# Performance work log

Hardware: AMD Instinct MI355X
Metric: run time of the kernel (lower is better)

Reference implementation:

```python
import jax, jax.numpy as jnp
import numpy as np

B, K, C, H, W = 16, 32, 256, 80, 80
NH, HD = 8, 32          # num_heads, head_dim (C = NH*HD)
S = 4                   # fixed roi_align sampling grid per 1x1 output bin
EPS = 1e-5


def _bn(x, g, b, m, v):
    # inference-mode BatchNorm2d, NCHW
    s = g / jnp.sqrt(v + EPS)
    return x * s[None, :, None, None] + (b - m * s)[None, :, None, None]


def _bilinear(feat, ys, xs):
    # feat [B,C,H,W]; ys,xs [B,K,S,S] -> [B,K,S,S,C], torchvision roi_align semantics
    Hh, Ww = feat.shape[2], feat.shape[3]
    valid = (ys >= -1.0) & (ys <= Hh) & (xs >= -1.0) & (xs <= Ww)
    y = jnp.clip(ys, 0.0, Hh - 1.0)
    x = jnp.clip(xs, 0.0, Ww - 1.0)
    y0 = jnp.floor(y); x0 = jnp.floor(x)
    y0i = y0.astype(jnp.int32); x0i = x0.astype(jnp.int32)
    y1i = jnp.minimum(y0i + 1, Hh - 1); x1i = jnp.minimum(x0i + 1, Ww - 1)
    ly = y - y0; lx = x - x0; hy = 1.0 - ly; hx = 1.0 - lx
    bidx = jnp.arange(feat.shape[0])[:, None, None, None]
    g = lambda yi, xi: feat[bidx, :, yi, xi]  # -> [B,K,S,S,C]
    val = ((hy * hx)[..., None] * g(y0i, x0i) + (hy * lx)[..., None] * g(y0i, x1i)
           + (ly * hx)[..., None] * g(y1i, x0i) + (ly * lx)[..., None] * g(y1i, x1i))
    return val * valid[..., None].astype(val.dtype)


def _roi_align_1x1(feat, boxes):
    # boxes [B,K,4] normalized xyxy; spatial_scale = 1.0 in the source
    Hh, Ww = feat.shape[2], feat.shape[3]
    sc = jnp.asarray([Ww - 1, Hh - 1, Ww - 1, Hh - 1], feat.dtype)
    ab = boxes * sc
    x1, y1, x2, y2 = ab[..., 0], ab[..., 1], ab[..., 2], ab[..., 3]
    rw = jnp.maximum(x2 - x1, 1.0)
    rh = jnp.maximum(y2 - y1, 1.0)
    grid = (jnp.arange(S, dtype=feat.dtype) + 0.5) / S
    ys = y1[..., None] + grid * rh[..., None]   # [B,K,S]
    xs = x1[..., None] + grid * rw[..., None]
    ys2, xs2 = jnp.broadcast_arrays(ys[..., :, None], xs[..., None, :])  # [B,K,S,S]
    vals = _bilinear(feat, ys2, xs2)            # [B,K,S,S,C]
    return vals.mean(axis=(2, 3)).reshape(feat.shape[0] * boxes.shape[1], -1)


def _gat(nodes, wq, bq, wk, bkp, wv, bv, scale, wo, bo, ln_g, ln_b):
    Bk = nodes.shape[0]
    q = (nodes @ wq.T + bq).reshape(Bk, NH, HD)
    k = (nodes @ wk.T + bkp).reshape(Bk, NH, HD)
    v = (nodes @ wv.T + bv).reshape(Bk, NH, HD)
    scores = jnp.einsum('ihd,jhd->ijh', q, k) * scale
    attn = jax.nn.softmax(scores, axis=1)       # softmax over keys j
    msg = jnp.einsum('ijh,jhd->ihd', attn, v).reshape(Bk, NH * HD)
    y = nodes + msg @ wo.T + bo
    mu = y.mean(-1, keepdims=True)
    var = ((y - mu) ** 2).mean(-1, keepdims=True)
    return (y - mu) / jnp.sqrt(var + EPS) * ln_g + ln_b


def _forward(x, boxes, conv_w, conv_b, bn1_g, bn1_b, bn1_m, bn1_v,
             wq, bq, wk, bkp, wv, bv, scale, wo, bo, ln_g, ln_b,
             rec_w, rec_b, bn2_g, bn2_b, bn2_m, bn2_v):
    feat = jax.lax.conv_general_dilated(
        x, conv_w, (1, 1), 'SAME',
        dimension_numbers=('NCHW', 'OIHW', 'NCHW')) + conv_b[None, :, None, None]
    feat = _bn(feat, bn1_g, bn1_b, bn1_m, bn1_v)
    feat = feat * jax.nn.sigmoid(feat)          # SiLU
    nodes = _roi_align_1x1(feat, boxes)         # [B*K, C]
    enh = _gat(nodes, wq, bq, wk, bkp, wv, bv, scale, wo, bo, ln_g, ln_b)
    f = enh.reshape(B, K, C)
    wts = jax.nn.softmax(f.mean(-1), axis=1)    # [B,K]
    weighted = jnp.einsum('bkc,bk->bc', f, wts)
    # out map is spatially constant -> 1x1 conv + BN collapse to per-sample affine
    y = weighted @ rec_w[:, :, 0, 0].T + rec_b
    s = bn2_g / jnp.sqrt(bn2_v + EPS)
    y = y * s + (bn2_b - bn2_m * s)
    return x + y[:, :, None, None]


def setup_inputs() -> dict:
    key = jax.random.key(0)
    ks = jax.random.split(key, 10)
    x = jax.random.normal(ks[0], (B, C, H, W), jnp.float32)
    bx = jax.random.uniform(ks[1], (B, K, 4), jnp.float32)
    bx = bx.at[:, :, 2:].add(bx[:, :, :2])      # xy2 += xy1
    boxes = jnp.clip(bx, 0.0, 1.0)
    w = lambda k, shp: jax.random.normal(k, shp, jnp.float32) * 0.02
    return {
        'x': x, 'boxes': boxes,
        'conv_w': w(ks[2], (C, C, 3, 3)), 'conv_b': jnp.zeros((C,), jnp.float32),
        'bn1_g': jnp.ones((C,), jnp.float32), 'bn1_b': jnp.zeros((C,), jnp.float32),
        'bn1_m': jnp.zeros((C,), jnp.float32), 'bn1_v': jnp.ones((C,), jnp.float32),
        'wq': w(ks[3], (C, C)), 'bq': jnp.zeros((C,), jnp.float32),
        'wk': w(ks[4], (C, C)), 'bkp': jnp.zeros((C,), jnp.float32),
        'wv': w(ks[5], (C, C)), 'bv': jnp.zeros((C,), jnp.float32),
        'scale': jnp.asarray(1.0 / np.sqrt(HD), jnp.float32),
        'wo': w(ks[6], (C, C)), 'bo': jnp.zeros((C,), jnp.float32),
        'ln_g': jnp.ones((C,), jnp.float32), 'ln_b': jnp.zeros((C,), jnp.float32),
        'rec_w': w(ks[7], (C, C, 1, 1)), 'rec_b': jnp.zeros((C,), jnp.float32),
        'bn2_g': jnp.ones((C,), jnp.float32), 'bn2_b': jnp.zeros((C,), jnp.float32),
        'bn2_m': jnp.zeros((C,), jnp.float32), 'bn2_v': jnp.ones((C,), jnp.float32),
    }


def reference(x, boxes, conv_w, conv_b, bn1_g, bn1_b, bn1_m, bn1_v,
              wq, bq, wk, bkp, wv, bv, scale, wo, bo, ln_g, ln_b,
              rec_w, rec_b, bn2_g, bn2_b, bn2_m, bn2_v):
    return _forward(x, boxes, conv_w, conv_b, bn1_g, bn1_b, bn1_m, bn1_v,
                    wq, bq, wk, bkp, wv, bv, scale, wo, bo, ln_g, ln_b,
                    rec_w, rec_b, bn2_g, bn2_b, bn2_m, bn2_v)
```

## Files before the change

### kernel.cpp

```cpp
#include <hip/hip_runtime.h>

#define EPSV 1e-5f

typedef __attribute__((ext_vector_type(8))) short short8v;
typedef __attribute__((ext_vector_type(4))) float f32x4;

static __device__ __forceinline__ unsigned short f2bf(float f) {
  unsigned int u = __float_as_uint(f);
  u += 0x7fff + ((u >> 16) & 1);
  return (unsigned short)(u >> 16);
}
static __device__ __forceinline__ float bf2f(unsigned short h) {
  return __uint_as_float(((unsigned int)h) << 16);
}

static __device__ __forceinline__ void glds16(const void* g, void* l) {
  __builtin_amdgcn_global_load_lds(
      (const __attribute__((address_space(1))) void*)g,
      (__attribute__((address_space(3))) void*)l, 16, 0, 0);
}

__global__ __launch_bounds__(256) void prep_fused_kernel(
    const float* __restrict__ x, unsigned short* __restrict__ xin,
    const float* __restrict__ cw, unsigned short* __restrict__ Wr,
    float* __restrict__ zpad,
    const float* __restrict__ wq, const float* __restrict__ wk,
    const float* __restrict__ wv, const float* __restrict__ wo,
    const float* __restrict__ rec, float* __restrict__ wT)
{
  __shared__ unsigned short t[80 * 257];
  const int bid = blockIdx.x;
  if (bid < 1280) {
    int b = bid / 80, y = bid - b * 80;
    const float* src = x + (size_t)b * 256 * 6400 + y * 80;
    for (int e = threadIdx.x; e < 256 * 20; e += 256) {
      int c = e / 20;
      int px4 = e - c * 20;
      f32x4 v = *(const f32x4*)&src[(size_t)c * 6400 + px4 * 4];
#pragma unroll
      for (int j = 0; j < 4; ++j)
        t[(px4 * 4 + j) * 257 + c] = f2bf(v[j]);
    }
    __syncthreads();
    unsigned short* dst = xin + (size_t)bid * 80 * 256;
    for (int e = threadIdx.x; e < 80 * 32; e += 256) {
      int px = e >> 5;
      int c8 = e & 31;
      short8v v;
#pragma unroll
      for (int j = 0; j < 8; ++j) v[j] = t[px * 257 + c8 * 8 + j];
      *(short8v*)&dst[px * 256 + c8 * 8] = v;
    }
  } else if (bid < 3584) {
    if (bid == 1280) zpad[threadIdx.x] = 0.f;
    int idx = (bid - 1280) * 256 + threadIdx.x;
    int cil = idx & 31;
    int rest = idx >> 5;
    int co = rest & 255;
    int tcc = rest >> 8;
    int cc = tcc & 7;
    int tt = tcc >> 3;
    int dy = tt / 3, dx = tt - dy * 3;
    int ci = cc * 32 + cil;
    Wr[idx] = f2bf(cw[((co * 256 + ci) * 3 + dy) * 3 + dx]);
  } else {
    int idx = (bid - 3584) * 256 + threadIdx.x;
    int m = idx >> 16;
    int e = idx & 65535;
    int ci = e >> 8, co = e & 255;
    const float* src = (m == 0) ? wq : (m == 1) ? wk : (m == 2) ? wv
                     : (m == 3) ? wo : rec;
    wT[idx] = src[co * 256 + ci];
  }
}

__global__ __launch_bounds__(256, 3) void roiconv_kernel(
    const unsigned short* __restrict__ xin,
    const float* __restrict__ boxes,
    const float* __restrict__ convb,
    const float* __restrict__ bn1g, const float* __restrict__ bn1b,
    const float* __restrict__ bn1m, const float* __restrict__ bn1v,
    const unsigned short* __restrict__ Wr,
    float* __restrict__ nodes)
{
  const int bid = blockIdx.x;
  const int n = (bid & 7) * 64 + (bid >> 3);
  const int b = n >> 5;
  const int tid = threadIdx.x;
  const int w = tid >> 6, lane = tid & 63;
  const int bq = lane >> 4, r16 = lane & 15;

  __shared__ __align__(16) char lds[41216];
  float* wcoef = (float*)(lds + 40960);
  const int IN0 = 0, IN1 = 4096, W0 = 8192, W1 = 24576;

  const int px = tid >> 2;
  const float* bx = boxes + n * 4;
  float x1 = bx[0] * 79.f, y1 = bx[1] * 79.f, x2 = bx[2] * 79.f, y2 = bx[3] * 79.f;
  float rwd = fmaxf(x2 - x1, 1.f), rh = fmaxf(y2 - y1, 1.f);
  int s = px >> 2;
  int sy = s >> 2, sx = s & 3;
  float yy = y1 + (sy + 0.5f) * 0.25f * rh;
  float xx = x1 + (sx + 0.5f) * 0.25f * rwd;
  bool valid = (yy >= -1.f) && (yy <= 80.f) && (xx >= -1.f) && (xx <= 80.f);
  float yc = fminf(fmaxf(yy, 0.f), 79.f), xc = fminf(fmaxf(xx, 0.f), 79.f);
  float y0f = floorf(yc), x0f = floorf(xc);
  int y0i = (int)y0f, x0i = (int)x0f;
  int y1i = min(y0i + 1, 79), x1i = min(x0i + 1, 79);
  float ly = yc - y0f, lx = xc - x0f, hy = 1.f - ly, hx = 1.f - lx;
  int py = (px & 2) ? y1i : y0i;
  int pxx = (px & 1) ? x1i : x0i;
  if ((tid & 3) == 0)
    wcoef[px] = ((px & 2) ? ly : hy) * ((px & 1) ? lx : hx) *
                (valid ? 0.0625f : 0.f);

  const int chunk = (tid & 3) ^ ((px >> 1) & 3);
  unsigned ioff[9];
#pragma unroll
  for (int t = 0; t < 9; ++t) {
    int dy = t / 3, dx = t - dy * 3;
    int cy = py + dy - 1, cx = pxx + dx - 1;
    bool ok = ((unsigned)cy < 80u) && ((unsigned)cx < 80u);
    ioff[t] = ok ? (unsigned)((((b * 80 + cy) * 80 + cx) * 256 + chunk * 8) * 2)
                 : 52428800u;
  }
  unsigned woff[4];
#pragma unroll
  for (int i = 0; i < 4; ++i) {
    int s2 = tid + (i << 8);
    int wco = s2 >> 2;
    int wch = (s2 & 3) ^ ((wco >> 1) & 3);
    woff[i] = (unsigned)((wco * 32 + wch * 8) * 2);
  }
  const int laneoff = r16 * 64 + ((bq ^ ((r16 >> 1) & 3)) << 4);
  const char* xinb = (const char*)xin;
  const char* Wrb = (const char*)Wr;

  f32x4 acc[4][4];
#pragma unroll
  for (int i = 0; i < 4; ++i)
#pragma unroll
    for (int j = 0; j < 4; ++j)
      acc[i][j] = (f32x4){0.f, 0.f, 0.f, 0.f};

  glds16(xinb + ioff[0], lds + IN0 + ((w << 6) << 4));
#pragma unroll
  for (int i = 0; i < 4; ++i)
    glds16(Wrb + woff[i], lds + W0 + (((i << 8) + (w << 6)) << 4));
  __syncthreads();

  for (int cc = 0; cc < 8; ++cc) {
#pragma unroll
    for (int t = 0; t < 9; ++t) {
      const int step = cc * 9 + t;
      const char* inb = lds + ((step & 1) ? IN1 : IN0);
      const char* wb  = lds + ((step & 1) ? W1 : W0);
      char* innx = lds + ((step & 1) ? IN0 : IN1);
      char* wbn  = lds + ((step & 1) ? W0 : W1);
      if (step < 71) {
        const int nt = (t == 8) ? 0 : t + 1;
        const int ncc = (t == 8) ? cc + 1 : cc;
        glds16(xinb + ioff[nt] + ncc * 64, innx + ((w << 6) << 4));
        const char* wg = Wrb + ((size_t)(nt * 8 + ncc) << 14);
#pragma unroll
        for (int i = 0; i < 4; ++i)
          glds16(wg + woff[i], wbn + (((i << 8) + (w << 6)) << 4));
      }
      const char* pa = inb + laneoff;
      const char* pw = wb + w * 4096 + laneoff;
      short8v af0 = *(const short8v*)(pa);
      short8v af1 = *(const short8v*)(pa + 1024);
      short8v af2 = *(const short8v*)(pa + 2048);
      short8v af3 = *(const short8v*)(pa + 3072);
      short8v wf0 = *(const short8v*)(pw);
      short8v wf1 = *(const short8v*)(pw + 1024);
      short8v wf2 = *(const short8v*)(pw + 2048);
      short8v wf3 = *(const short8v*)(pw + 3072);
      __builtin_amdgcn_s_setprio(1);
      acc[0][0] = __builtin_amdgcn_mfma_f32_16x16x32_bf16(af0, wf0, acc[0][0], 0, 0, 0);
      acc[0][1] = __builtin_amdgcn_mfma_f32_16x16x32_bf16(af0, wf1, acc[0][1], 0, 0, 0);
      acc[0][2] = __builtin_amdgcn_mfma_f32_16x16x32_bf16(af0, wf2, acc[0][2], 0, 0, 0);
      acc[0][3] = __builtin_amdgcn_mfma_f32_16x16x32_bf16(af0, wf3, acc[0][3], 0, 0, 0);
      acc[1][0] = __builtin_amdgcn_mfma_f32_16x16x32_bf16(af1, wf0, acc[1][0], 0, 0, 0);
      acc[1][1] = __builtin_amdgcn_mfma_f32_16x16x32_bf16(af1, wf1, acc[1][1], 0, 0, 0);
      acc[1][2] = __builtin_amdgcn_mfma_f32_16x16x32_bf16(af1, wf2, acc[1][2], 0, 0, 0);
      acc[1][3] = __builtin_amdgcn_mfma_f32_16x16x32_bf16(af1, wf3, acc[1][3], 0, 0, 0);
      acc[2][0] = __builtin_amdgcn_mfma_f32_16x16x32_bf16(af2, wf0, acc[2][0], 0, 0, 0);
      acc[2][1] = __builtin_amdgcn_mfma_f32_16x16x32_bf16(af2, wf1, acc[2][1], 0, 0, 0);
      acc[2][2] = __builtin_amdgcn_mfma_f32_16x16x32_bf16(af2, wf2, acc[2][2], 0, 0, 0);
      acc[2][3] = __builtin_amdgcn_mfma_f32_16x16x32_bf16(af2, wf3, acc[2][3], 0, 0, 0);
      acc[3][0] = __builtin_amdgcn_mfma_f32_16x16x32_bf16(af3, wf0, acc[3][0], 0, 0, 0);
      acc[3][1] = __builtin_amdgcn_mfma_f32_16x16x32_bf16(af3, wf1, acc[3][1], 0, 0, 0);
      acc[3][2] = __builtin_amdgcn_mfma_f32_16x16x32_bf16(af3, wf2, acc[3][2], 0, 0, 0);
      acc[3][3] = __builtin_amdgcn_mfma_f32_16x16x32_bf16(af3, wf3, acc[3][3], 0, 0, 0);
      __builtin_amdgcn_s_setprio(0);
      __syncthreads();
    }
  }

  unsigned short* ep = (unsigned short*)lds;
#pragma unroll
  for (int cf = 0; cf < 4; ++cf) {
    int co = w * 64 + cf * 16 + r16;
    float sc = bn1g[co] / sqrtf(bn1v[co] + EPSV);
    float sh = bn1b[co] - bn1m[co] * sc;
    float cb = convb[co];
#pragma unroll
    for (int mf = 0; mf < 4; ++mf) {
#pragma unroll
      for (int rg = 0; rg < 4; ++rg) {
        int pxo = mf * 16 + bq * 4 + rg;
        float v = (acc[mf][cf][rg] + cb) * sc + sh;
        v = v / (1.f + __expf(-v));
        ep[pxo * 264 + co] = f2bf(v);
      }
    }
  }
  __syncthreads();
  const int c = tid;
  float val = 0.f;
#pragma unroll
  for (int p = 0; p < 64; ++p)
    val += wcoef[p] * bf2f(ep[p * 264 + c]);
  nodes[n * 256 + c] = val;
}

__global__ __launch_bounds__(256) void qkv_kernel(
    const float* __restrict__ nodes, const float* __restrict__ wT,
    const float* __restrict__ bq, const float* __restrict__ bk,
    const float* __restrict__ bv,
    float* __restrict__ q, float* __restrict__ k, float* __restrict__ v)
{
  const int blk = blockIdx.x;
  const int co = threadIdx.x;
  __shared__ float nd[8][256];
  for (int i = threadIdx.x; i < 2048; i += 256)
    nd[i >> 8][i & 255] = nodes[blk * 2048 + i];
  __syncthreads();
  float aq[8] = {0,0,0,0,0,0,0,0};
  float ak[8] = {0,0,0,0,0,0,0,0};
  float av[8] = {0,0,0,0,0,0,0,0};
  const float* wqT = wT;
  const float* wkT = wT + 65536;
  const float* wvT = wT + 131072;
  for (int ci = 0; ci < 256; ++ci) {
    float wq_ = wqT[ci * 256 + co];
    float wk_ = wkT[ci * 256 + co];
    float wv_ = wvT[ci * 256 + co];
#pragma unroll
    for (int r = 0; r < 8; ++r) {
      float nv = nd[r][ci];
      aq[r] += nv * wq_;
      ak[r] += nv * wk_;
      av[r] += nv * wv_;
    }
  }
  float bq_ = bq[co], bk_ = bk[co], bv_ = bv[co];
#pragma unroll
  for (int r = 0; r < 8; ++r) {
    int n = blk * 8 + r;
    q[n * 256 + co] = aq[r] + bq_;
    k[n * 256 + co] = ak[r] + bk_;
    v[n * 256 + co] = av[r] + bv_;
  }
}

__global__ __launch_bounds__(256) void attn_mh_kernel(
    const float* __restrict__ q, const float* __restrict__ k,
    const float* __restrict__ v, const float* __restrict__ scale_p,
    float* __restrict__ msgs)
{
  const int bid = blockIdx.x;
  const int h = bid & 7, qc = bid >> 3;
  const int q0 = qc * 16;
  const int tid = threadIdx.x;
  __shared__ __align__(16) float Kh[512 * 32];
  __shared__ __align__(16) float Vh[512 * 32];
  __shared__ unsigned short pb[16 * 512];

  for (int idx = tid; idx < 4096; idx += 256) {
    int j = idx >> 3, part = idx & 7;
    int chs = part ^ (j & 7);
    *(f32x4*)&Kh[j * 32 + chs * 4] =
        *(const f32x4*)&k[(size_t)j * 256 + h * 32 + part * 4];
    *(f32x4*)&Vh[j * 32 + chs * 4] =
        *(const f32x4*)&v[(size_t)j * 256 + h * 32 + part * 4];
  }
  const int qi = tid >> 4, l = tid & 15;
  f32x4 qr[8];
#pragma unroll
  for (int p = 0; p < 8; ++p)
    qr[p] = *(const f32x4*)&q[(size_t)(q0 + qi) * 256 + h * 32 + p * 4];
  const float scale = scale_p[0];
  __syncthreads();

  float pj[32];
  float mx = -1e30f;
#pragma unroll
  for (int jj = 0; jj < 32; ++jj) {
    int j = jj * 16 + l;
    const float* kr = &Kh[j * 32];
    int sw = j & 7;
    float s = 0.f;
#pragma unroll
    for (int p = 0; p < 8; ++p) {
      f32x4 kv = *(const f32x4*)&kr[(p ^ sw) * 4];
      s += kv.x * qr[p].x + kv.y * qr[p].y + kv.z * qr[p].z + kv.w * qr[p].w;
    }
    s *= scale;
    pj[jj] = s;
    mx = fmaxf(mx, s);
  }
#pragma unroll
  for (int o = 1; o < 16; o <<= 1) mx = fmaxf(mx, __shfl_xor(mx, o, 16));
  float sum = 0.f;
#pragma unroll
  for (int jj = 0; jj < 32; ++jj) {
    float e = __expf(pj[jj] - mx);
    pj[jj] = e;
    sum += e;
  }
#pragma unroll
  for (int o = 1; o < 16; o <<= 1) sum += __shfl_xor(sum, o, 16);
  float inv = 1.f / sum;
#pragma unroll
  for (int jj = 0; jj < 32; ++jj)
    pb[qi * 512 + jj * 16 + l] = f2bf(pj[jj] * inv);
  __syncthreads();

  float m0 = 0.f, m1 = 0.f;
  const unsigned short* pq = &pb[qi * 512];
  for (int j = 0; j < 512; ++j) {
    float p = bf2f(pq[j]);
    int chs = (l >> 1) ^ (j & 7);
    const float* vr = &Vh[j * 32 + chs * 4 + ((2 * l) & 3)];
    m0 += p * vr[0];
    m1 += p * vr[1];
  }
  float* mo = &msgs[(size_t)(q0 + qi) * 256 + h * 32 + 2 * l];
  mo[0] = m0;
  mo[1] = m1;
}

__global__ __launch_bounds__(256) void outln_kernel(
    const float* __restrict__ msgs, const float* __restrict__ nodes,
    const float* __restrict__ woT, const float* __restrict__ bo,
    const float* __restrict__ lng, const float* __restrict__ lnb,
    float* __restrict__ enh)
{
  const int blk = blockIdx.x;
  const int co = threadIdx.x;
  __shared__ float ms[8][256];
  __shared__ float red1[8][4], red2[8][4];
  for (int i = co; i < 2048; i += 256)
    ms[i >> 8][i & 255] = msgs[blk * 2048 + i];
  __syncthreads();
  float yv[8];
  float bo_ = bo[co];
#pragma unroll
  for (int r = 0; r < 8; ++r)
    yv[r] = nodes[(size_t)(blk * 8 + r) * 256 + co] + bo_;
  for (int ci = 0; ci < 256; ++ci) {
    float w = woT[ci * 256 + co];
#pragma unroll
    for (int r = 0; r < 8; ++r) yv[r] += ms[r][ci] * w;
  }
  const int wv = co >> 6, lane = co & 63;
#pragma unroll
  for (int r = 0; r < 8; ++r) {
    float s1 = yv[r], s2 = yv[r] * yv[r];
#pragma unroll
    for (int o = 1; o < 64; o <<= 1) {
      s1 += __shfl_xor(s1, o);
      s2 += __shfl_xor(s2, o);
    }
    if (lane == 0) { red1[r][wv] = s1; red2[r][wv] = s2; }
  }
  __syncthreads();
  float lg = lng[co], lb = lnb[co];
#pragma unroll
  for (int r = 0; r < 8; ++r) {
    float S1 = red1[r][0] + red1[r][1] + red1[r][2] + red1[r][3];
    float S2 = red2[r][0] + red2[r][1] + red2[r][2] + red2[r][3];
    float mu = S1 * (1.f / 256.f);
    float var = S2 * (1.f / 256.f) - mu * mu;
    enh[(size_t)(blk * 8 + r) * 256 + co] =
        (yv[r] - mu) * rsqrtf(var + EPSV) * lg + lb;
  }
}

__global__ __launch_bounds__(256) void final_kernel(
    const float* __restrict__ enh, const float* __restrict__ recT,
    const float* __restrict__ recb,
    const float* __restrict__ bn2g, const float* __restrict__ bn2b,
    const float* __restrict__ bn2m, const float* __restrict__ bn2v,
    float* __restrict__ yfin)
{
  const int b = blockIdx.x;
  const int tid = threadIdx.x;
  const int wv = tid >> 6, l = tid & 63;
  __shared__ float rm[32], wts[32], wgt[256];
  for (int kk = wv; kk < 32; kk += 4) {
    const float* er = enh + (size_t)(b * 32 + kk) * 256;
    float s = er[l] + er[l + 64] + er[l + 128] + er[l + 192];
#pragma unroll
    for (int o = 1; o < 64; o <<= 1) s += __shfl_xor(s, o);
    if (l == 0) rm[kk] = s * (1.f / 256.f);
  }
  __syncthreads();
  if (tid < 32) {
    float m = rm[tid];
    float mx = m;
#pragma unroll
    for (int o = 1; o < 32; o <<= 1) mx = fmaxf(mx, __shfl_xor(mx, o, 32));
    float e = __expf(m - mx);
    float sm = e;
#pragma unroll
    for (int o = 1; o < 32; o <<= 1) sm += __shfl_xor(sm, o, 32);
    wts[tid] = e / sm;
  }
  __syncthreads();
  float wsum = 0.f;
  for (int kk = 0; kk < 32; ++kk)
    wsum += enh[(size_t)(b * 32 + kk) * 256 + tid] * wts[kk];
  wgt[tid] = wsum;
  __syncthreads();
  const int co = tid;
  float yv = recb[co];
  for (int ci = 0; ci < 256; ++ci)
    yv += wgt[ci] * recT[ci * 256 + co];
  float s = bn2g[co] / sqrtf(bn2v[co] + EPSV);
  yfin[b * 256 + co] = yv * s + (bn2b[co] - bn2m[co] * s);
}

__global__ __launch_bounds__(256) void add_kernel(
    const float* __restrict__ x, const float* __restrict__ yfin,
    float* __restrict__ out)
{
  const int bc = blockIdx.x;
  const float a = yfin[bc];
  const f32x4* xp = (const f32x4*)(x + (size_t)bc * 6400);
  f32x4* op = (f32x4*)(out + (size_t)bc * 6400);
  for (int i = threadIdx.x; i < 1600; i += 256) {
    f32x4 v = xp[i];
    v.x += a; v.y += a; v.z += a; v.w += a;
    op[i] = v;
  }
}

extern "C" void kernel_launch(void* const* d_in, const int* in_sizes, int n_in,
                              void* d_out, int out_size, void* d_ws, size_t ws_size,
                              hipStream_t stream)
{
  const float* x      = (const float*)d_in[0];
  const float* boxes  = (const float*)d_in[1];
  const float* conv_w = (const float*)d_in[2];
  const float* conv_b = (const float*)d_in[3];
  const float* bn1g   = (const float*)d_in[4];
  const float* bn1b   = (const float*)d_in[5];
  const float* bn1m   = (const float*)d_in[6];
  const float* bn1v   = (const float*)d_in[7];
  const float* wq     = (const float*)d_in[8];
  const float* bq     = (const float*)d_in[9];
  const float* wk     = (const float*)d_in[10];
  const float* bkp    = (const float*)d_in[11];
  const float* wv     = (const float*)d_in[12];
  const float* bv     = (const float*)d_in[13];
  const float* scale  = (const float*)d_in[14];
  const float* wo     = (const float*)d_in[15];
  const float* bo     = (const float*)d_in[16];
  const float* lng    = (const float*)d_in[17];
  const float* lnb    = (const float*)d_in[18];
  const float* rec_w  = (const float*)d_in[19];
  const float* rec_b  = (const float*)d_in[20];
  const float* bn2g   = (const float*)d_in[21];
  const float* bn2b   = (const float*)d_in[22];
  const float* bn2m   = (const float*)d_in[23];
  const float* bn2v   = (const float*)d_in[24];
  float* out = (float*)d_out;

  char* ws = (char*)d_ws;
  unsigned short* Wr = (unsigned short*)(ws);
  float* wT    = (float*)(ws + 53608448);
  float* nodes = (float*)(ws + 54919168);
  float* qb    = nodes + 131072;
  float* kb    = qb + 131072;
  float* vb    = kb + 131072;
  float* enh   = vb + 131072;
  float* yfin  = enh + 131072;
  float* msgs  = yfin + 4096;

  unsigned short* xin = (unsigned short*)d_out;
  float* zpad = (float*)((char*)d_out + 52428800);

  hipLaunchKernelGGL(prep_fused_kernel, dim3(4864), dim3(256), 0, stream,
                     x, xin, conv_w, Wr, zpad, wq, wk, wv, wo, rec_w, wT);
  hipLaunchKernelGGL(roiconv_kernel, dim3(512), dim3(256), 0, stream,
                     xin, boxes, conv_b, bn1g, bn1b, bn1m, bn1v, Wr, nodes);
  hipLaunchKernelGGL(qkv_kernel, dim3(64), dim3(256), 0, stream,
                     nodes, wT, bq, bkp, bv, qb, kb, vb);
  hipLaunchKernelGGL(attn_mh_kernel, dim3(256), dim3(256), 0, stream,
                     qb, kb, vb, scale, msgs);
  hipLaunchKernelGGL(outln_kernel, dim3(64), dim3(256), 0, stream,
                     msgs, nodes, wT + 3 * 65536, bo, lng, lnb, enh);
  hipLaunchKernelGGL(final_kernel, dim3(16), dim3(256), 0, stream,
                     enh, wT + 4 * 65536, rec_b, bn2g, bn2b, bn2m, bn2v, yfin);
  hipLaunchKernelGGL(add_kernel, dim3(4096), dim3(256), 0, stream, x, yfin, out);
}
```

Baseline: 190.1 us.

## Triple-buffer roiconv loads with vmcnt waits and split qkv into more blocks

The roiconv main loop moves from a double buffer to a triple buffer in LDS, prefetching two steps ahead. The per-step __syncthreads is replaced by a partial s_waitcnt vmcnt plus a raw barrier, so global-to-LDS loads can overlap more of the MFMA work. LDS use grows to about 60 KB and launch bounds drop to 2 blocks per CU, which lowers occupancy. Separately, qkv_kernel now handles 4 rows per block across 128 blocks instead of 8 rows across 64, to use more CUs.

```diff
diff --git a/kernel.cpp b/kernel.cpp
--- a/kernel.cpp
+++ b/kernel.cpp
@@ -74,7 +74,7 @@
   }
 }
 
-__global__ __launch_bounds__(256, 3) void roiconv_kernel(
+__global__ __launch_bounds__(256, 2) void roiconv_kernel(
     const unsigned short* __restrict__ xin,
     const float* __restrict__ boxes,
     const float* __restrict__ convb,
@@ -90,9 +90,8 @@
   const int w = tid >> 6, lane = tid & 63;
   const int bq = lane >> 4, r16 = lane & 15;
 
-  __shared__ __align__(16) char lds[41216];
-  float* wcoef = (float*)(lds + 40960);
-  const int IN0 = 0, IN1 = 4096, W0 = 8192, W1 = 24576;
+  __shared__ __align__(16) char lds[61696];
+  float* wcoef = (float*)(lds + 61440);
 
   const int px = tid >> 2;
   const float* bx = boxes + n * 4;
@@ -135,6 +134,7 @@
   const int laneoff = r16 * 64 + ((bq ^ ((r16 >> 1) & 3)) << 4);
   const char* xinb = (const char*)xin;
   const char* Wrb = (const char*)Wr;
+  const int ldst_in = (w << 6) << 4;
 
   f32x4 acc[4][4];
 #pragma unroll
@@ -143,24 +143,35 @@
     for (int j = 0; j < 4; ++j)
       acc[i][j] = (f32x4){0.f, 0.f, 0.f, 0.f};
 
-  glds16(xinb + ioff[0], lds + IN0 + ((w << 6) << 4));
+  glds16(xinb + ioff[0], lds + 0 + ldst_in);
 #pragma unroll
   for (int i = 0; i < 4; ++i)
-    glds16(Wrb + woff[i], lds + W0 + (((i << 8) + (w << 6)) << 4));
-  __syncthreads();
+    glds16(Wrb + woff[i], lds + 12288 + (((i << 8) + (w << 6)) << 4));
+  glds16(xinb + ioff[1], lds + 4096 + ldst_in);
+#pragma unroll
+  for (int i = 0; i < 4; ++i)
+    glds16(Wrb + ((size_t)8 << 14) + woff[i],
+           lds + 28672 + (((i << 8) + (w << 6)) << 4));
 
   for (int cc = 0; cc < 8; ++cc) {
 #pragma unroll
     for (int t = 0; t < 9; ++t) {
-      const int step = cc * 9 + t;
-      const char* inb = lds + ((step & 1) ? IN1 : IN0);
-      const char* wb  = lds + ((step & 1) ? W1 : W0);
-      char* innx = lds + ((step & 1) ? IN0 : IN1);
-      char* wbn  = lds + ((step & 1) ? W0 : W1);
-      if (step < 71) {
-        const int nt = (t == 8) ? 0 : t + 1;
-        const int ncc = (t == 8) ? cc + 1 : cc;
-        glds16(xinb + ioff[nt] + ncc * 64, innx + ((w << 6) << 4));
+      const int cb = t % 3;
+      const char* inb = lds + cb * 4096;
+      const char* wb  = lds + 12288 + cb * 16384;
+      if (cc == 7 && t == 8)
+        asm volatile("s_waitcnt vmcnt(0)" ::: "memory");
+      else
+        asm volatile("s_waitcnt vmcnt(5)" ::: "memory");
+      __builtin_amdgcn_s_barrier();
+      __builtin_amdgcn_sched_barrier(0);
+      if (!(cc == 7 && t >= 7)) {
+        const int nt = (t + 2 > 8) ? t - 7 : t + 2;
+        const int nb = nt % 3;
+        const int ncc = cc + (t >= 7 ? 1 : 0);
+        char* innx = lds + nb * 4096;
+        char* wbn  = lds + 12288 + nb * 16384;
+        glds16(xinb + ioff[nt] + ncc * 64, innx + ldst_in);
         const char* wg = Wrb + ((size_t)(nt * 8 + ncc) << 14);
 #pragma unroll
         for (int i = 0; i < 4; ++i)
@@ -194,9 +205,10 @@
       acc[3][2] = __builtin_amdgcn_mfma_f32_16x16x32_bf16(af3, wf2, acc[3][2], 0, 0, 0);
       acc[3][3] = __builtin_amdgcn_mfma_f32_16x16x32_bf16(af3, wf3, acc[3][3], 0, 0, 0);
       __builtin_amdgcn_s_setprio(0);
-      __syncthreads();
-    }
-  }
+    }
+  }
+  asm volatile("s_waitcnt vmcnt(0)" ::: "memory");
+  __syncthreads();
 
   unsigned short* ep = (unsigned short*)lds;
 #pragma unroll
@@ -233,13 +245,13 @@
 {
   const int blk = blockIdx.x;
   const int co = threadIdx.x;
-  __shared__ float nd[8][256];
-  for (int i = threadIdx.x; i < 2048; i += 256)
-    nd[i >> 8][i & 255] = nodes[blk * 2048 + i];
-  __syncthreads();
-  float aq[8] = {0,0,0,0,0,0,0,0};
-  float ak[8] = {0,0,0,0,0,0,0,0};
-  float av[8] = {0,0,0,0,0,0,0,0};
+  __shared__ float nd[4][256];
+  for (int i = threadIdx.x; i < 1024; i += 256)
+    nd[i >> 8][i & 255] = nodes[blk * 1024 + i];
+  __syncthreads();
+  float aq[4] = {0, 0, 0, 0};
+  float ak[4] = {0, 0, 0, 0};
+  float av[4] = {0, 0, 0, 0};
   const float* wqT = wT;
   const float* wkT = wT + 65536;
   const float* wvT = wT + 131072;
@@ -248,7 +260,7 @@
     float wk_ = wkT[ci * 256 + co];
     float wv_ = wvT[ci * 256 + co];
 #pragma unroll
-    for (int r = 0; r < 8; ++r) {
+    for (int r = 0; r < 4; ++r) {
       float nv = nd[r][ci];
       aq[r] += nv * wq_;
       ak[r] += nv * wk_;
@@ -257,8 +269,8 @@
   }
   float bq_ = bq[co], bk_ = bk[co], bv_ = bv[co];
 #pragma unroll
-  for (int r = 0; r < 8; ++r) {
-    int n = blk * 8 + r;
+  for (int r = 0; r < 4; ++r) {
+    int n = blk * 4 + r;
     q[n * 256 + co] = aq[r] + bq_;
     k[n * 256 + co] = ak[r] + bk_;
     v[n * 256 + co] = av[r] + bv_;
@@ -497,7 +509,7 @@
                      x, xin, conv_w, Wr, zpad, wq, wk, wv, wo, rec_w, wT);
   hipLaunchKernelGGL(roiconv_kernel, dim3(512), dim3(256), 0, stream,
                      xin, boxes, conv_b, bn1g, bn1b, bn1m, bn1v, Wr, nodes);
-  hipLaunchKernelGGL(qkv_kernel, dim3(64), dim3(256), 0, stream,
+  hipLaunchKernelGGL(qkv_kernel, dim3(128), dim3(256), 0, stream,
                      nodes, wT, bq, bkp, bv, qb, kb, vb);
   hipLaunchKernelGGL(attn_mh_kernel, dim3(256), dim3(256), 0, stream,
                      qb, kb, vb, scale, msgs);
```

New measurement: 186.7 us. About the same (-1.8%).
